# Optimization experiments

Measured on AMD Instinct MI355X. Metric: run time of the kernel, lower is better.

## Reference

```python
import jax, jax.numpy as jnp
import numpy as np

ALPHA = 0.2      # LeakyReLU negative slope
NEG_INF = -9e15  # mask value from the original code

def setup_inputs() -> dict:
    key = jax.random.key(0)
    k1, k2, k3, k4 = jax.random.split(key, 4)
    B, M, F_IN, F_OUT = 16, 2048, 128, 64
    h = jax.random.normal(k1, (B, M, F_IN), dtype=jnp.float32)
    adj = jax.random.randint(k2, (B, M, M), 0, 2, dtype=jnp.int32)
    W = jax.random.normal(k3, (F_IN, F_OUT), dtype=jnp.float32) * 0.1
    a = jax.random.normal(k4, (2 * F_OUT, 1), dtype=jnp.float32) * 0.1
    return {"h": h, "adj": adj, "W": W, "a": a}

def reference(h, adj, W, a):
    # h: [B,M,Fin], adj: [B,M,M], W: [Fin,E], a: [2E,1]
    Wh = jnp.matmul(h, W)                      # [B,M,E]
    E = Wh.shape[-1]
    a1, a2 = a[:E, 0], a[E:, 0]
    # decompose a^T [Wh_i || Wh_j] = (Wh_i . a1) + (Wh_j . a2)
    f1 = Wh @ a1                               # [B,M] (source/query term)
    f2 = Wh @ a2                               # [B,M] (target/key term)
    e = jax.nn.leaky_relu(f1[:, :, None] + f2[:, None, :], negative_slope=ALPHA)  # [B,M,M]
    scores = jnp.where(adj > 0, e, NEG_INF)
    attn = jax.nn.softmax(scores, axis=-1)     # [B,M,M]  (dropout p=0 / eval mode)
    h_prime = jnp.matmul(attn, Wh)             # [B,M,E]
    return jax.nn.elu(h_prime)                 # concat=True branch
```

## Files before the change

### kernel.cpp

```cpp
#include <hip/hip_runtime.h>


#define M_     2048
#define FIN_   128
#define F_     64
#define ALPHA_ 0.2f
#define HS_    132
#define WT_    132

typedef float  float4_ __attribute__((ext_vector_type(4)));
typedef short  short8  __attribute__((ext_vector_type(8)));
typedef int    int4_   __attribute__((ext_vector_type(4)));
typedef unsigned int u32x4 __attribute__((ext_vector_type(4)));
typedef unsigned short u16;
typedef unsigned int   u32;

static __device__ __forceinline__ u32 cvtpk(float lo, float hi) {
    u32 r;
    asm("v_cvt_pk_bf16_f32 %0, %1, %2" : "=v"(r) : "v"(lo), "v"(hi));
    return r;
}

static __device__ __forceinline__ int4_ ntload4(const int* p) {
    return __builtin_nontemporal_load((const int4_*)p);
}

__global__ __launch_bounds__(256, 4) void k_prep(
    const float* __restrict__ h, const float* __restrict__ W,
    const float* __restrict__ a, u16* __restrict__ hbf,
    float* __restrict__ f1all, float* __restrict__ f2all)
{
    __shared__ float a_s[2 * F_];
    __shared__ float wa1[FIN_], wa2[FIN_];
    __shared__ float hs[32 * HS_];

    const int tid = threadIdx.x;
    const u32 bid = blockIdx.x;
    const u32 lg  = (bid & 7) * 128 + (bid >> 3);
    const int b   = lg >> 6;
    const int t   = lg & 63;

    if (tid < 128) a_s[tid] = a[tid];

    const int tok = tid >> 3, f0 = (tid & 7) * 16;
    const float* hp = h + ((size_t)(b * M_ + t * 32 + tok)) * FIN_ + f0;
    float4_ x0 = *(const float4_*)hp;
    float4_ x1 = *(const float4_*)(hp + 4);
    float4_ x2 = *(const float4_*)(hp + 8);
    float4_ x3 = *(const float4_*)(hp + 12);
    __syncthreads();

    if (tid < FIN_) {
        float s1 = 0.f, s2 = 0.f;
#pragma unroll 8
        for (int n = 0; n < F_; ++n) {
            float wv = W[tid * F_ + n];
            s1 += wv * a_s[n];
            s2 += wv * a_s[F_ + n];
        }
        wa1[tid] = s1;
        wa2[tid] = s2;
    }

    float* hr = hs + tok * HS_ + f0;
    *(float4_*)(hr)      = x0;
    *(float4_*)(hr + 4)  = x1;
    *(float4_*)(hr + 8)  = x2;
    *(float4_*)(hr + 12) = x3;
    __syncthreads();

    {
        const int l = tid & 63, lc = l & 15, q = l >> 4;
        const int nt0 = (tid >> 6) * 2;
        u32x4* ob = (u32x4*)hbf + ((size_t)(b * 64 + t)) * 8 * 64;
#pragma unroll
        for (int ni = 0; ni < 2; ++ni) {
            const int nt = nt0 + ni;
            const float* cp = hs + (q * 8) * HS_ + nt * 16 + lc;
            u32x4 wv;
            wv[0] = cvtpk(cp[0 * HS_], cp[1 * HS_]);
            wv[1] = cvtpk(cp[2 * HS_], cp[3 * HS_]);
            wv[2] = cvtpk(cp[4 * HS_], cp[5 * HS_]);
            wv[3] = cvtpk(cp[6 * HS_], cp[7 * HS_]);
            ob[nt * 64 + l] = wv;
        }
    }

    {
        const int r = tid >> 3, k0 = (tid & 7) * 16;
        const float* rp = hs + r * HS_ + k0;
        float s1 = 0.f, s2 = 0.f;
#pragma unroll
        for (int k = 0; k < 16; ++k) {
            s1 += rp[k] * wa1[k0 + k];
            s2 += rp[k] * wa2[k0 + k];
        }
        s1 += __shfl_xor(s1, 1, 64); s2 += __shfl_xor(s2, 1, 64);
        s1 += __shfl_xor(s1, 2, 64); s2 += __shfl_xor(s2, 2, 64);
        s1 += __shfl_xor(s1, 4, 64); s2 += __shfl_xor(s2, 4, 64);
        if ((tid & 7) == 0) {
            f1all[b * M_ + t * 32 + r] = s1;
            f2all[b * M_ + t * 32 + r] = s2;
        }
    }
}

__global__ __launch_bounds__(256, 4) void k_main(
    const int* __restrict__ adj, const u16* __restrict__ hbf,
    const float* __restrict__ f1all, const float* __restrict__ f2all,
    const float* __restrict__ W, float* __restrict__ out)
{
    __shared__ char  dyn[WT_ * 32 * 4];
    __shared__ float dens2[64];

    float* f2s  = (float*)dyn;
    float* Tsum = (float*)dyn;

    const int tid  = threadIdx.x;
    const int w    = tid >> 6;
    const int l    = tid & 63;
    const int lc   = l & 15;
    const int quad = l >> 4;
    const int wr   = w & 1;
    const int wh   = w >> 1;

    const u32 bid = blockIdx.x;
    const u32 lg  = (bid & 7) * 128 + (bid >> 3);
    const int b   = lg >> 6;
    const int i0  = (lg & 63) * 32;
    const int rowbase = i0 + wr * 16;

    {
        const int o = tid * 8;
        float4_ v0 = *(const float4_*)(f2all + b * M_ + o);
        float4_ v1 = *(const float4_*)(f2all + b * M_ + o + 4);
        *(float4_*)(f2s + o)     = v0;
        *(float4_*)(f2s + o + 4) = v1;
    }

    const float f1r = f1all[b * M_ + rowbase + lc];
    const int* aprow = adj + ((size_t)(b * M_ + rowbase + lc)) * M_ + quad * 8;
    const u32x4* hb  = (const u32x4*)hbf + ((size_t)b * 64) * 8 * 64 + l;

    const int t0 = wh * 32;
    const int tE = t0 + 31;

    int4_ aA0 = ntload4(aprow + t0 * 32);
    int4_ aA1 = ntload4(aprow + t0 * 32 + 4);
    int4_ aB0 = ntload4(aprow + (t0 + 1) * 32);
    int4_ aB1 = ntload4(aprow + (t0 + 1) * 32 + 4);

    __syncthreads();

    float denacc = 0.f;
    float4_ acc[8];
#pragma unroll
    for (int nt = 0; nt < 8; ++nt) acc[nt] = (float4_){0.f, 0.f, 0.f, 0.f};

#define SC(GE, GO, AE, AO, IDX)                                 \
        {                                                       \
            float xe = f1r + (GE); xe = fmaxf(xe, ALPHA_ * xe); \
            float xo = f1r + (GO); xo = fmaxf(xo, ALPHA_ * xo); \
            float ee = ((AE) > 0) ? __expf(xe) : 0.f;           \
            float eo = ((AO) > 0) ? __expf(xo) : 0.f;           \
            u32 pk = cvtpk(ee, eo);                             \
            d += __uint_as_float(pk << 16);                     \
            d += __uint_as_float(pk & 0xFFFF0000u);             \
            pw[IDX] = pk;                                       \
        }

#define STAGE(T, A0, A1)                                                      \
    {                                                                         \
        const int tp = ((T) + 2 <= tE) ? (T) + 2 : tE;                        \
        u32x4 bb[8];                                                          \
        _Pragma("unroll")                                                     \
        for (int nt = 0; nt < 8; ++nt) bb[nt] = hb[((T) * 8 + nt) * 64];      \
        float4_ g0 = *(const float4_*)(f2s + (T) * 32 + quad * 8);            \
        float4_ g1 = *(const float4_*)(f2s + (T) * 32 + quad * 8 + 4);        \
        u32x4 pw;                                                             \
        float d = 0.f;                                                        \
        SC(g0[0], g0[1], A0[0], A0[1], 0)                                     \
        SC(g0[2], g0[3], A0[2], A0[3], 1)                                     \
        SC(g1[0], g1[1], A1[0], A1[1], 2)                                     \
        SC(g1[2], g1[3], A1[2], A1[3], 3)                                     \
        denacc += d;                                                          \
        const short8 af = __builtin_bit_cast(short8, pw);                     \
        A0 = ntload4(aprow + tp * 32);                                        \
        A1 = ntload4(aprow + tp * 32 + 4);                                    \
        _Pragma("unroll")                                                     \
        for (int nt = 0; nt < 8; ++nt)                                        \
            acc[nt] = __builtin_amdgcn_mfma_f32_16x16x32_bf16(                \
                af, __builtin_bit_cast(short8, bb[nt]), acc[nt], 0, 0, 0);    \
    }

    for (int o = 0; o < 16; ++o) {
        STAGE(t0 + 2 * o,     aA0, aA1)
        STAGE(t0 + 2 * o + 1, aB0, aB1)
    }
#undef STAGE
#undef SC

    denacc += __shfl_xor(denacc, 16, 64);
    denacc += __shfl_xor(denacc, 32, 64);
    if (quad == 0) dens2[wh * 32 + wr * 16 + lc] = denacc;
    __syncthreads();

    if (wh == 0) {
#pragma unroll
        for (int nt = 0; nt < 8; ++nt)
#pragma unroll
            for (int mm = 0; mm < 4; ++mm)
                Tsum[(wr * 16 + quad * 4 + mm) * WT_ + nt * 16 + lc] = acc[nt][mm];
    }
    __syncthreads();
    if (wh == 1) {
#pragma unroll
        for (int nt = 0; nt < 8; ++nt)
#pragma unroll
            for (int mm = 0; mm < 4; ++mm)
                Tsum[(wr * 16 + quad * 4 + mm) * WT_ + nt * 16 + lc] += acc[nt][mm];
    }
    __syncthreads();

    {
        const int r  = tid >> 3;
        const int n0 = (tid & 7) * 8;
        const float den  = dens2[r] + dens2[32 + r];
        const float rden = (den > 0.f) ? (1.f / den) : 0.f;
        float u[8];
#pragma unroll
        for (int nn = 0; nn < 8; ++nn) u[nn] = 0.f;
#pragma unroll 4
        for (int k = 0; k < FIN_; ++k) {
            const float tv = Tsum[r * WT_ + k];
            float4_ wv0 = *(const float4_*)(W + k * F_ + n0);
            float4_ wv1 = *(const float4_*)(W + k * F_ + n0 + 4);
            u[0] += tv * wv0[0]; u[1] += tv * wv0[1];
            u[2] += tv * wv0[2]; u[3] += tv * wv0[3];
            u[4] += tv * wv1[0]; u[5] += tv * wv1[1];
            u[6] += tv * wv1[2]; u[7] += tv * wv1[3];
        }
        float4_ o0, o1;
#pragma unroll
        for (int nn = 0; nn < 8; ++nn) {
            float hp = u[nn] * rden;
            float o  = hp > 0.f ? hp : expm1f(hp);
            if (nn < 4) o0[nn] = o; else o1[nn - 4] = o;
        }
        float* op = out + ((size_t)(b * M_ + i0 + r)) * F_ + n0;
        *(float4_*)op       = o0;
        *(float4_*)(op + 4) = o1;
    }
}

extern "C" void kernel_launch(void* const* d_in, const int* in_sizes, int n_in,
                              void* d_out, int out_size, void* d_ws, size_t ws_size,
                              hipStream_t stream)
{
    (void)out_size; (void)ws_size;
    const float* h  = (const float*)d_in[0];
    const int* adjp = (const int*)d_in[1];
    const float* Wp = (const float*)d_in[2];
    const float* ap = (const float*)d_in[3];
    for (int i = 0; i < n_in; ++i) {
        long s = in_sizes[i];
        if      (s == 4194304L)  h    = (const float*)d_in[i];
        else if (s == 67108864L) adjp = (const int*)d_in[i];
        else if (s == 8192L)     Wp   = (const float*)d_in[i];
        else if (s == 128L)      ap   = (const float*)d_in[i];
    }
    u16*   hbf   = (u16*)d_ws;
    float* f1all = (float*)((char*)d_ws + (8u << 20));
    float* f2all = f1all + 16 * M_;
    k_prep<<<1024, 256, 0, stream>>>(h, Wp, ap, hbf, f1all, f2all);
    k_main<<<1024, 256, 0, stream>>>(adjp, hbf, f1all, f2all, Wp, (float*)d_out);
}
```

Before: 445.0 us.

## Split score computation into separate kernel writing bf16 MFMA-layout probabilities

```diff
diff --git a/kernel.cpp b/kernel.cpp
--- a/kernel.cpp
+++ b/kernel.cpp
@@ -12,6 +12,7 @@
 typedef short  short8  __attribute__((ext_vector_type(8)));
 typedef int    int4_   __attribute__((ext_vector_type(4)));
 typedef unsigned int u32x4 __attribute__((ext_vector_type(4)));
+typedef unsigned int u32x2 __attribute__((ext_vector_type(2)));
 typedef unsigned short u16;
 typedef unsigned int   u32;
 
@@ -105,16 +106,49 @@
     }
 }
 
+__global__ __launch_bounds__(256, 4) void k_score(
+    const int* __restrict__ adj, const float* __restrict__ f1all,
+    const float* __restrict__ f2all, u16* __restrict__ P)
+{
+    const u32 stride = 2048 * 256;
+    u32 e = blockIdx.x * 256 + threadIdx.x;
+#pragma unroll 2
+    for (int it = 0; it < 32; ++it, e += stride) {
+        const u32 b  = e >> 20;
+        const u32 l4 = e & 511;
+
+        int4_ c4 = ntload4(adj + (size_t)e * 4);
+        const float f1v = f1all[e >> 9];
+        float4_ g = *(const float4_*)(f2all + (b << 11) + l4 * 4);
+
+        float x0 = f1v + g[0]; x0 = fmaxf(x0, ALPHA_ * x0);
+        float x1 = f1v + g[1]; x1 = fmaxf(x1, ALPHA_ * x1);
+        float x2 = f1v + g[2]; x2 = fmaxf(x2, ALPHA_ * x2);
+        float x3 = f1v + g[3]; x3 = fmaxf(x3, ALPHA_ * x3);
+        float e0 = (c4[0] > 0) ? __expf(x0) : 0.f;
+        float e1 = (c4[1] > 0) ? __expf(x1) : 0.f;
+        float e2 = (c4[2] > 0) ? __expf(x2) : 0.f;
+        float e3 = (c4[3] > 0) ? __expf(x3) : 0.f;
+        u32x2 pk;
+        pk[0] = cvtpk(e0, e1);
+        pk[1] = cvtpk(e2, e3);
+
+        const u32 row  = (e >> 9) & 2047;
+        const u32 rg   = row >> 4, lc = row & 15;
+        const u32 tile = l4 >> 3;
+        const u32 quad = (l4 >> 1) & 3;
+        const u32 half = l4 & 1;
+        const u32 pe   = ((((b << 7) + rg) << 6) + tile) * 64 + (lc << 2) + quad;
+        *(u32x2*)((u32*)(P + (size_t)pe * 8) + half * 2) = pk;
+    }
+}
+
 __global__ __launch_bounds__(256, 4) void k_main(
-    const int* __restrict__ adj, const u16* __restrict__ hbf,
-    const float* __restrict__ f1all, const float* __restrict__ f2all,
+    const u16* __restrict__ P, const u16* __restrict__ hbf,
     const float* __restrict__ W, float* __restrict__ out)
 {
-    __shared__ char  dyn[WT_ * 32 * 4];
+    __shared__ float Tsum[32 * WT_];
     __shared__ float dens2[64];
-
-    float* f2s  = (float*)dyn;
-    float* Tsum = (float*)dyn;
 
     const int tid  = threadIdx.x;
     const int w    = tid >> 6;
@@ -128,77 +162,41 @@
     const u32 lg  = (bid & 7) * 128 + (bid >> 3);
     const int b   = lg >> 6;
     const int i0  = (lg & 63) * 32;
-    const int rowbase = i0 + wr * 16;
-
-    {
-        const int o = tid * 8;
-        float4_ v0 = *(const float4_*)(f2all + b * M_ + o);
-        float4_ v1 = *(const float4_*)(f2all + b * M_ + o + 4);
-        *(float4_*)(f2s + o)     = v0;
-        *(float4_*)(f2s + o + 4) = v1;
-    }
-
-    const float f1r = f1all[b * M_ + rowbase + lc];
-    const int* aprow = adj + ((size_t)(b * M_ + rowbase + lc)) * M_ + quad * 8;
-    const u32x4* hb  = (const u32x4*)hbf + ((size_t)b * 64) * 8 * 64 + l;
+    const int rgw = (lg & 63) * 2 + wr;
+
+    const u32x4* pb = (const u32x4*)P
+                    + (((size_t)((b << 7) + rgw)) << 12) + (lc << 2) + quad;
+    const u32x4* hb = (const u32x4*)hbf + ((size_t)b * 64) * 8 * 64 + l;
 
     const int t0 = wh * 32;
-    const int tE = t0 + 31;
-
-    int4_ aA0 = ntload4(aprow + t0 * 32);
-    int4_ aA1 = ntload4(aprow + t0 * 32 + 4);
-    int4_ aB0 = ntload4(aprow + (t0 + 1) * 32);
-    int4_ aB1 = ntload4(aprow + (t0 + 1) * 32 + 4);
-
-    __syncthreads();
 
     float denacc = 0.f;
     float4_ acc[8];
 #pragma unroll
     for (int nt = 0; nt < 8; ++nt) acc[nt] = (float4_){0.f, 0.f, 0.f, 0.f};
 
-#define SC(GE, GO, AE, AO, IDX)                                 \
-        {                                                       \
-            float xe = f1r + (GE); xe = fmaxf(xe, ALPHA_ * xe); \
-            float xo = f1r + (GO); xo = fmaxf(xo, ALPHA_ * xo); \
-            float ee = ((AE) > 0) ? __expf(xe) : 0.f;           \
-            float eo = ((AO) > 0) ? __expf(xo) : 0.f;           \
-            u32 pk = cvtpk(ee, eo);                             \
-            d += __uint_as_float(pk << 16);                     \
-            d += __uint_as_float(pk & 0xFFFF0000u);             \
-            pw[IDX] = pk;                                       \
-        }
-
-#define STAGE(T, A0, A1)                                                      \
-    {                                                                         \
-        const int tp = ((T) + 2 <= tE) ? (T) + 2 : tE;                        \
-        u32x4 bb[8];                                                          \
-        _Pragma("unroll")                                                     \
-        for (int nt = 0; nt < 8; ++nt) bb[nt] = hb[((T) * 8 + nt) * 64];      \
-        float4_ g0 = *(const float4_*)(f2s + (T) * 32 + quad * 8);            \
-        float4_ g1 = *(const float4_*)(f2s + (T) * 32 + quad * 8 + 4);        \
-        u32x4 pw;                                                             \
-        float d = 0.f;                                                        \
-        SC(g0[0], g0[1], A0[0], A0[1], 0)                                     \
-        SC(g0[2], g0[3], A0[2], A0[3], 1)                                     \
-        SC(g1[0], g1[1], A1[0], A1[1], 2)                                     \
-        SC(g1[2], g1[3], A1[2], A1[3], 3)                                     \
-        denacc += d;                                                          \
-        const short8 af = __builtin_bit_cast(short8, pw);                     \
-        A0 = ntload4(aprow + tp * 32);                                        \
-        A1 = ntload4(aprow + tp * 32 + 4);                                    \
-        _Pragma("unroll")                                                     \
-        for (int nt = 0; nt < 8; ++nt)                                        \
-            acc[nt] = __builtin_amdgcn_mfma_f32_16x16x32_bf16(                \
-                af, __builtin_bit_cast(short8, bb[nt]), acc[nt], 0, 0, 0);    \
-    }
-
-    for (int o = 0; o < 16; ++o) {
-        STAGE(t0 + 2 * o,     aA0, aA1)
-        STAGE(t0 + 2 * o + 1, aB0, aB1)
-    }
-#undef STAGE
-#undef SC
+    for (int k = 0; k < 32; ++k) {
+        const int t = t0 + k;
+
+        u32x4 pv = pb[(size_t)t << 6];
+        u32x4 bb[8];
+#pragma unroll
+        for (int nt = 0; nt < 8; ++nt) bb[nt] = hb[(t * 8 + nt) * 64];
+
+        float d = 0.f;
+#pragma unroll
+        for (int kk = 0; kk < 4; ++kk) {
+            d += __uint_as_float(pv[kk] << 16);
+            d += __uint_as_float(pv[kk] & 0xFFFF0000u);
+        }
+        denacc += d;
+
+        const short8 af = __builtin_bit_cast(short8, pv);
+#pragma unroll
+        for (int nt = 0; nt < 8; ++nt)
+            acc[nt] = __builtin_amdgcn_mfma_f32_16x16x32_bf16(
+                af, __builtin_bit_cast(short8, bb[nt]), acc[nt], 0, 0, 0);
+    }
 
     denacc += __shfl_xor(denacc, 16, 64);
     denacc += __shfl_xor(denacc, 32, 64);
@@ -272,6 +270,8 @@
     u16*   hbf   = (u16*)d_ws;
     float* f1all = (float*)((char*)d_ws + (8u << 20));
     float* f2all = f1all + 16 * M_;
-    k_prep<<<1024, 256, 0, stream>>>(h, Wp, ap, hbf, f1all, f2all);
-    k_main<<<1024, 256, 0, stream>>>(adjp, hbf, f1all, f2all, Wp, (float*)d_out);
-}
+    u16*   Pp    = (u16*)((char*)d_ws + (16u << 20));
+    k_prep <<<1024, 256, 0, stream>>>(h, Wp, ap, hbf, f1all, f2all);
+    k_score<<<2048, 256, 0, stream>>>(adjp, f1all, f2all, Pp);
+    k_main <<<1024, 256, 0, stream>>>(Pp, hbf, Wp, (float*)d_out);
+}
```

Result: slower. 475.9 us (+7.0%).
